# Optimization experiments

Hardware: AMD Instinct MI355X
Metric: run time of the kernel (lower is better)

Reference implementation:

```python
import jax, jax.numpy as jnp
import numpy as np

WS = 7        # window_size
SHIFT = 3     # shift_size
HEADS = 6
DIM = 192
HIDDEN = DIM * 6  # mlp_ratio=6
EPS = 1e-5


def _rel_pos_index(ws):
    # static relative-position index, (ws*ws, ws*ws) int
    coords = np.stack(np.meshgrid(np.arange(ws), np.arange(ws), indexing='ij')).reshape(2, -1)
    rel = coords[:, :, None] - coords[:, None, :]            # (2, N, N)
    rel = rel.transpose(1, 2, 0)                             # (N, N, 2)
    rel[:, :, 0] += ws - 1
    rel[:, :, 1] += ws - 1
    rel[:, :, 0] *= 2 * ws - 1
    return rel.sum(-1)


def _layernorm(t, g, b):
    m = t.mean(-1, keepdims=True)
    v = jnp.mean((t - m) ** 2, axis=-1, keepdims=True)
    return (t - m) * jax.lax.rsqrt(v + EPS) * g + b


def setup_inputs() -> dict:
    key = jax.random.key(0)
    ks = jax.random.split(key, 8)
    B, H, W = 16, 56, 56
    x = jax.random.normal(ks[0], (B, H * W, DIM), dtype=jnp.float32)
    p = lambda k, s: (jax.random.normal(k, s, dtype=jnp.float32) * 0.02)
    return {
        'x': x, 'H': H, 'W': W,
        'ln1_g': jnp.ones((DIM,), jnp.float32), 'ln1_b': jnp.zeros((DIM,), jnp.float32),
        'qkv_w': p(ks[1], (3 * DIM, DIM)), 'qkv_b': jnp.zeros((3 * DIM,), jnp.float32),
        'rpb': p(ks[2], ((2 * WS - 1) ** 2, HEADS)),
        'proj_w': p(ks[3], (DIM, DIM)), 'proj_b': jnp.zeros((DIM,), jnp.float32),
        'ln2_g': jnp.ones((DIM,), jnp.float32), 'ln2_b': jnp.zeros((DIM,), jnp.float32),
        'fc1_w': p(ks[4], (HIDDEN, DIM)), 'fc1_b': jnp.zeros((HIDDEN,), jnp.float32),
        'fc2_w': p(ks[5], (DIM, HIDDEN)), 'fc2_b': jnp.zeros((DIM,), jnp.float32),
    }


def reference(x, H, W, ln1_g, ln1_b, qkv_w, qkv_b, rpb, proj_w, proj_b,
              ln2_g, ln2_b, fc1_w, fc1_b, fc2_w, fc2_b):
    B, L, C = x.shape
    hd = C // HEADS
    shortcut = x
    h = _layernorm(x, ln1_g, ln1_b).reshape(B, H, W, C)
    pad_r = (WS - W % WS) % WS
    pad_b = (WS - H % WS) % WS
    h = jnp.pad(h, ((0, 0), (0, pad_b), (0, pad_r), (0, 0)))
    Hp, Wp = H + pad_b, W + pad_r
    if SHIFT > 0:
        h = jnp.roll(h, (-SHIFT, -SHIFT), axis=(1, 2))
    # window partition -> (nW*B, WS*WS, C)
    h = h.reshape(B, Hp // WS, WS, Wp // WS, WS, C).transpose(0, 1, 3, 2, 4, 5)
    h = h.reshape(-1, WS * WS, C)
    nB, N, _ = h.shape
    qkv = (h @ qkv_w.T + qkv_b).reshape(nB, N, 3, HEADS, hd).transpose(2, 0, 3, 1, 4)
    q, k, v = qkv[0], qkv[1], qkv[2]       # (nB, heads, N, hd)
    scale = hd ** -0.5
    attn = jnp.einsum('bhnd,bhmd->bhnm', q * scale, k)
    idx = _rel_pos_index(WS)
    bias = rpb[idx.reshape(-1)].reshape(N, N, HEADS).transpose(2, 0, 1)  # (heads, N, N)
    attn = jax.nn.softmax(attn + bias[None], axis=-1)
    out = jnp.einsum('bhnm,bhmd->bhnd', attn, v).transpose(0, 2, 1, 3).reshape(nB, N, C)
    out = out @ proj_w.T + proj_b
    # window reverse -> (B, Hp, Wp, C)
    out = out.reshape(B, Hp // WS, Wp // WS, WS, WS, C).transpose(0, 1, 3, 2, 4, 5)
    out = out.reshape(B, Hp, Wp, C)
    if SHIFT > 0:
        out = jnp.roll(out, (SHIFT, SHIFT), axis=(1, 2))
    out = out[:, :H, :W, :].reshape(B, H * W, C)
    x = shortcut + out
    h2 = _layernorm(x, ln2_g, ln2_b)
    h2 = jax.nn.gelu(h2 @ fc1_w.T + fc1_b, approximate=False)
    return x + (h2 @ fc2_w.T + fc2_b)
```

## Files before the change

kernel.cpp:

```cpp
#include <hip/hip_runtime.h>

typedef unsigned short u16;
typedef __bf16 bf16x8 __attribute__((ext_vector_type(8)));
typedef float f32x4 __attribute__((ext_vector_type(4)));

__device__ __forceinline__ u16 f2bf(float f) {
  union { float f; unsigned int u; } v; v.f = f;
  unsigned int u = v.u;
  u += 0x7fffu + ((u >> 16) & 1u);
  return (u16)(u >> 16);
}
__device__ __forceinline__ float bf2f(u16 h) {
  union { unsigned int u; float f; } v; v.u = ((unsigned int)h) << 16; return v.f;
}

__global__ __launch_bounds__(256) void cast_weights(
    const float* __restrict__ w0, const float* __restrict__ w1,
    const float* __restrict__ w2, const float* __restrict__ w3,
    u16* __restrict__ o0, u16* __restrict__ o1,
    u16* __restrict__ o2, u16* __restrict__ o3) {
  int i = blockIdx.x * 256 + threadIdx.x;
  if (i < 110592) o0[i] = f2bf(w0[i]);
  if (i < 36864)  o1[i] = f2bf(w1[i]);
  if (i < 221184) o2[i] = f2bf(w2[i]);
  if (i < 221184) o3[i] = f2bf(w3[i]);
}

__global__ __launch_bounds__(256) void ln_kernel(
    const float* __restrict__ x, const float* __restrict__ g,
    const float* __restrict__ b, u16* __restrict__ out) {
  int row = blockIdx.x * 4 + (threadIdx.x >> 6);
  int lane = threadIdx.x & 63;
  const float* xr = x + (long)row * 192;
  float e0 = xr[lane], e1 = xr[lane + 64], e2 = xr[lane + 128];
  float s = e0 + e1 + e2;
  #pragma unroll
  for (int o = 1; o < 64; o <<= 1) s += __shfl_xor(s, o);
  float mean = s * (1.0f / 192.0f);
  float d0 = e0 - mean, d1 = e1 - mean, d2 = e2 - mean;
  float q = d0 * d0 + d1 * d1 + d2 * d2;
  #pragma unroll
  for (int o = 1; o < 64; o <<= 1) q += __shfl_xor(q, o);
  float rstd = rsqrtf(q * (1.0f / 192.0f) + 1e-5f);
  u16* orow = out + (long)row * 192;
  orow[lane]       = f2bf(d0 * rstd * g[lane]       + b[lane]);
  orow[lane + 64]  = f2bf(d1 * rstd * g[lane + 64]  + b[lane + 64]);
  orow[lane + 128] = f2bf(d2 * rstd * g[lane + 128] + b[lane + 128]);
}

template<int MODE>
__global__ __launch_bounds__(256) void gemm_kernel(
    const u16* __restrict__ A, const u16* __restrict__ W,
    const float* __restrict__ bias, const float* __restrict__ resid,
    void* __restrict__ out, int N, int K) {
  __shared__ u16 lA[128 * 40];
  __shared__ u16 lB[64 * 40];
  int tid = threadIdx.x;
  int wave = tid >> 6, lane = tid & 63;
  int wm = wave >> 1, wn = wave & 1;
  int quad = lane >> 4, l15 = lane & 15;
  long bm = (long)blockIdx.x * 128;
  int bn = blockIdx.y * 64;
  int r = tid >> 2, cg = (tid & 3) * 8;
  f32x4 acc[4][2] = {};
  for (int k0 = 0; k0 < K; k0 += 32) {
    uint4 a0 = *(const uint4*)(A + (bm + r) * K + k0 + cg);
    uint4 a1 = *(const uint4*)(A + (bm + 64 + r) * K + k0 + cg);
    uint4 b0 = *(const uint4*)(W + (long)(bn + r) * K + k0 + cg);
    __syncthreads();
    *(uint4*)&lA[r * 40 + cg] = a0;
    *(uint4*)&lA[(64 + r) * 40 + cg] = a1;
    *(uint4*)&lB[r * 40 + cg] = b0;
    __syncthreads();
    bf16x8 af[4], bfr[2];
    #pragma unroll
    for (int mt = 0; mt < 4; mt++)
      af[mt] = *(const bf16x8*)&lA[(wm * 64 + mt * 16 + l15) * 40 + quad * 8];
    #pragma unroll
    for (int nt = 0; nt < 2; nt++)
      bfr[nt] = *(const bf16x8*)&lB[(wn * 32 + nt * 16 + l15) * 40 + quad * 8];
    #pragma unroll
    for (int mt = 0; mt < 4; mt++)
      #pragma unroll
      for (int nt = 0; nt < 2; nt++)
        acc[mt][nt] = __builtin_amdgcn_mfma_f32_16x16x32_bf16(af[mt], bfr[nt], acc[mt][nt], 0, 0, 0);
  }
  #pragma unroll
  for (int mt = 0; mt < 4; mt++) {
    #pragma unroll
    for (int nt = 0; nt < 2; nt++) {
      int col = bn + wn * 32 + nt * 16 + l15;
      float bi = bias[col];
      #pragma unroll
      for (int j = 0; j < 4; j++) {
        long row = bm + wm * 64 + mt * 16 + quad * 4 + j;
        float v = acc[mt][nt][j] + bi;
        long idx = row * N + col;
        if (MODE == 0) {
          ((u16*)out)[idx] = f2bf(v);
        } else if (MODE == 1) {
          v = 0.5f * v * (1.0f + erff(v * 0.70710678118f));
          ((u16*)out)[idx] = f2bf(v);
        } else {
          ((float*)out)[idx] = resid[idx] + v;
        }
      }
    }
  }
}

__global__ __launch_bounds__(256) void attn_kernel(
    const u16* __restrict__ qkv, const float* __restrict__ rpb,
    u16* __restrict__ attn) {
  __shared__ float ql[49 * 36], kl[49 * 36], vl[49 * 36];
  __shared__ float S[49 * 52];
  __shared__ int rowmap[49];
  int tid = threadIdx.x;
  int win = blockIdx.x, head = blockIdx.y;
  int b = win >> 6, wy = (win >> 3) & 7, wx = win & 7;
  if (tid < 49) {
    int i = tid / 7, j = tid - i * 7;
    int y  = (wy * 7 + i + 3) % 56;
    int xx = (wx * 7 + j + 3) % 56;
    rowmap[tid] = b * 3136 + y * 56 + xx;
  }
  __syncthreads();
  const float scale = 0.17677669529663687f;
  for (int t = tid; t < 49 * 32; t += 256) {
    int n = t >> 5, d = t & 31;
    long base = (long)rowmap[n] * 576 + head * 32 + d;
    ql[n * 36 + d] = bf2f(qkv[base]) * scale;
    kl[n * 36 + d] = bf2f(qkv[base + 192]);
    vl[n * 36 + d] = bf2f(qkv[base + 384]);
  }
  __syncthreads();
  for (int e = tid; e < 49 * 49; e += 256) {
    int n = e / 49, m = e - n * 49;
    const float4* qp = (const float4*)&ql[n * 36];
    const float4* kp = (const float4*)&kl[m * 36];
    float s = 0.0f;
    #pragma unroll
    for (int d4 = 0; d4 < 8; d4++) {
      float4 a = qp[d4], bb = kp[d4];
      s += a.x * bb.x + a.y * bb.y + a.z * bb.z + a.w * bb.w;
    }
    int ni = n / 7, nj = n - ni * 7, mi = m / 7, mj = m - mi * 7;
    s += rpb[((ni - mi + 6) * 13 + (nj - mj + 6)) * 6 + head];
    S[n * 52 + m] = s;
  }
  __syncthreads();
  if (tid < 49) {
    float mx = -1e30f;
    for (int m = 0; m < 49; m++) mx = fmaxf(mx, S[tid * 52 + m]);
    float sum = 0.0f;
    for (int m = 0; m < 49; m++) {
      float e = __expf(S[tid * 52 + m] - mx);
      S[tid * 52 + m] = e; sum += e;
    }
    float inv = 1.0f / sum;
    for (int m = 0; m < 49; m++) S[tid * 52 + m] *= inv;
  }
  __syncthreads();
  for (int e = tid; e < 49 * 8; e += 256) {
    int n = e >> 3, d4 = (e & 7) * 4;
    float4 o = make_float4(0.f, 0.f, 0.f, 0.f);
    for (int m = 0; m < 49; m++) {
      float p = S[n * 52 + m];
      const float4 vv = *(const float4*)&vl[m * 36 + d4];
      o.x += p * vv.x; o.y += p * vv.y; o.z += p * vv.z; o.w += p * vv.w;
    }
    long gb = (long)rowmap[n] * 192 + head * 32 + d4;
    unsigned int p0 = (unsigned int)f2bf(o.x) | ((unsigned int)f2bf(o.y) << 16);
    unsigned int p1 = (unsigned int)f2bf(o.z) | ((unsigned int)f2bf(o.w) << 16);
    *(uint2*)&attn[gb] = make_uint2(p0, p1);
  }
}

extern "C" void kernel_launch(void* const* d_in, const int* in_sizes, int n_in,
                              void* d_out, int out_size, void* d_ws, size_t ws_size,
                              hipStream_t stream) {
  (void)in_sizes; (void)n_in; (void)out_size; (void)ws_size;
  const float* x      = (const float*)d_in[0];
  const float* ln1_g  = (const float*)d_in[3];
  const float* ln1_b  = (const float*)d_in[4];
  const float* qkv_w  = (const float*)d_in[5];
  const float* qkv_b  = (const float*)d_in[6];
  const float* rpb    = (const float*)d_in[7];
  const float* proj_w = (const float*)d_in[8];
  const float* proj_b = (const float*)d_in[9];
  const float* ln2_g  = (const float*)d_in[10];
  const float* ln2_b  = (const float*)d_in[11];
  const float* fc1_w  = (const float*)d_in[12];
  const float* fc1_b  = (const float*)d_in[13];
  const float* fc2_w  = (const float*)d_in[14];
  const float* fc2_b  = (const float*)d_in[15];

  char* ws = (char*)d_ws;
  float* x2   = (float*)(ws + 0);
  u16* hA     = (u16*)(ws + 38535168);
  u16* qkv    = (u16*)(ws + 57802752);
  u16* attn   = (u16*)(ws + 115605504);
  u16* hid    = (u16*)(ws + 57802752);
  u16* wbuf   = (u16*)(ws + 173408256);
  u16* qkv_wb = wbuf;
  u16* proj_wb = wbuf + 110592;
  u16* fc1_wb = wbuf + 147456;
  u16* fc2_wb = wbuf + 368640;

  cast_weights<<<dim3(864), 256, 0, stream>>>(qkv_w, proj_w, fc1_w, fc2_w,
                                              qkv_wb, proj_wb, fc1_wb, fc2_wb);
  ln_kernel<<<dim3(12544), 256, 0, stream>>>(x, ln1_g, ln1_b, hA);
  gemm_kernel<0><<<dim3(392, 9), 256, 0, stream>>>(hA, qkv_wb, qkv_b, nullptr,
                                                   qkv, 576, 192);
  attn_kernel<<<dim3(1024, 6), 256, 0, stream>>>(qkv, rpb, attn);
  gemm_kernel<2><<<dim3(392, 3), 256, 0, stream>>>(attn, proj_wb, proj_b, x,
                                                   x2, 192, 192);
  ln_kernel<<<dim3(12544), 256, 0, stream>>>(x2, ln2_g, ln2_b, hA);
  gemm_kernel<1><<<dim3(392, 18), 256, 0, stream>>>(hA, fc1_wb, fc1_b, nullptr,
                                                    hid, 1152, 192);
  gemm_kernel<2><<<dim3(392, 3), 256, 0, stream>>>(hid, fc2_wb, fc2_b, x2,
                                                   (float*)d_out, 192, 1152);
}
```

Baseline: 374.3 us.

## Rewrite window attention with MFMA per wave, precompute bias table, widen fc1 tiles

The window attention kernel now gives each wave one (window, head) pair. It computes QK^T and PV with bf16 MFMA instructions on tiles padded to 64, replacing the scalar fp32 dot products and the single-thread softmax. A small kernel precomputes a padded relative-position bias table per head, with -1e30 in the padded key slots, so the attention kernel no longer gathers rpb. The GEMM is templated on tile counts, and fc1 uses a 128x128 tile to halve its grid. Probabilities and V are kept in bf16, which lowers precision relative to the fp32 softmax path.

```diff
diff --git a/kernel.cpp b/kernel.cpp
--- a/kernel.cpp
+++ b/kernel.cpp
@@ -26,6 +26,23 @@
   if (i < 221184) o3[i] = f2bf(w3[i]);
 }
 
+__global__ __launch_bounds__(256) void build_btab(
+    const float* __restrict__ rpb, float* __restrict__ btab) {
+  int id = blockIdx.x * 256 + threadIdx.x;
+  int head = id >> 12;
+  int m = (id >> 6) & 63;
+  int r = id & 63;
+  float v;
+  if (m >= 49) v = -1e30f;
+  else if (r >= 49) v = 0.0f;
+  else {
+    int mi = m / 7, mj = m - mi * 7;
+    int ri = r / 7, rj = r - ri * 7;
+    v = rpb[((ri - mi + 6) * 13 + (rj - mj + 6)) * 6 + head];
+  }
+  btab[id] = v;
+}
+
 __global__ __launch_bounds__(256) void ln_kernel(
     const float* __restrict__ x, const float* __restrict__ g,
     const float* __restrict__ b, u16* __restrict__ out) {
@@ -48,52 +65,57 @@
   orow[lane + 128] = f2bf(d2 * rstd * g[lane + 128] + b[lane + 128]);
 }
 
-template<int MODE>
+template<int MODE, int MT, int NT>
 __global__ __launch_bounds__(256) void gemm_kernel(
     const u16* __restrict__ A, const u16* __restrict__ W,
     const float* __restrict__ bias, const float* __restrict__ resid,
     void* __restrict__ out, int N, int K) {
-  __shared__ u16 lA[128 * 40];
-  __shared__ u16 lB[64 * 40];
+  __shared__ u16 lA[MT * 32 * 40];
+  __shared__ u16 lB[NT * 32 * 40];
   int tid = threadIdx.x;
   int wave = tid >> 6, lane = tid & 63;
   int wm = wave >> 1, wn = wave & 1;
   int quad = lane >> 4, l15 = lane & 15;
-  long bm = (long)blockIdx.x * 128;
-  int bn = blockIdx.y * 64;
+  long bm = (long)blockIdx.x * (MT * 32);
+  int bn = blockIdx.y * (NT * 32);
   int r = tid >> 2, cg = (tid & 3) * 8;
-  f32x4 acc[4][2] = {};
+  f32x4 acc[MT][NT] = {};
   for (int k0 = 0; k0 < K; k0 += 32) {
-    uint4 a0 = *(const uint4*)(A + (bm + r) * K + k0 + cg);
-    uint4 a1 = *(const uint4*)(A + (bm + 64 + r) * K + k0 + cg);
-    uint4 b0 = *(const uint4*)(W + (long)(bn + r) * K + k0 + cg);
+    uint4 av[MT / 2], bv[NT / 2];
+    #pragma unroll
+    for (int i = 0; i < MT / 2; i++)
+      av[i] = *(const uint4*)(A + (bm + i * 64 + r) * K + k0 + cg);
+    #pragma unroll
+    for (int i = 0; i < NT / 2; i++)
+      bv[i] = *(const uint4*)(W + (long)(bn + i * 64 + r) * K + k0 + cg);
     __syncthreads();
-    *(uint4*)&lA[r * 40 + cg] = a0;
-    *(uint4*)&lA[(64 + r) * 40 + cg] = a1;
-    *(uint4*)&lB[r * 40 + cg] = b0;
+    #pragma unroll
+    for (int i = 0; i < MT / 2; i++) *(uint4*)&lA[(i * 64 + r) * 40 + cg] = av[i];
+    #pragma unroll
+    for (int i = 0; i < NT / 2; i++) *(uint4*)&lB[(i * 64 + r) * 40 + cg] = bv[i];
     __syncthreads();
-    bf16x8 af[4], bfr[2];
-    #pragma unroll
-    for (int mt = 0; mt < 4; mt++)
-      af[mt] = *(const bf16x8*)&lA[(wm * 64 + mt * 16 + l15) * 40 + quad * 8];
-    #pragma unroll
-    for (int nt = 0; nt < 2; nt++)
-      bfr[nt] = *(const bf16x8*)&lB[(wn * 32 + nt * 16 + l15) * 40 + quad * 8];
-    #pragma unroll
-    for (int mt = 0; mt < 4; mt++)
+    bf16x8 af[MT], bfr[NT];
+    #pragma unroll
+    for (int mt = 0; mt < MT; mt++)
+      af[mt] = *(const bf16x8*)&lA[(wm * (MT * 16) + mt * 16 + l15) * 40 + quad * 8];
+    #pragma unroll
+    for (int nt = 0; nt < NT; nt++)
+      bfr[nt] = *(const bf16x8*)&lB[(wn * (NT * 16) + nt * 16 + l15) * 40 + quad * 8];
+    #pragma unroll
+    for (int mt = 0; mt < MT; mt++)
       #pragma unroll
-      for (int nt = 0; nt < 2; nt++)
+      for (int nt = 0; nt < NT; nt++)
         acc[mt][nt] = __builtin_amdgcn_mfma_f32_16x16x32_bf16(af[mt], bfr[nt], acc[mt][nt], 0, 0, 0);
   }
   #pragma unroll
-  for (int mt = 0; mt < 4; mt++) {
-    #pragma unroll
-    for (int nt = 0; nt < 2; nt++) {
-      int col = bn + wn * 32 + nt * 16 + l15;
+  for (int mt = 0; mt < MT; mt++) {
+    #pragma unroll
+    for (int nt = 0; nt < NT; nt++) {
+      int col = bn + wn * (NT * 16) + nt * 16 + l15;
       float bi = bias[col];
       #pragma unroll
       for (int j = 0; j < 4; j++) {
-        long row = bm + wm * 64 + mt * 16 + quad * 4 + j;
+        long row = bm + wm * (MT * 16) + mt * 16 + quad * 4 + j;
         float v = acc[mt][nt][j] + bi;
         long idx = row * N + col;
         if (MODE == 0) {
@@ -110,69 +132,134 @@
 }
 
 __global__ __launch_bounds__(256) void attn_kernel(
-    const u16* __restrict__ qkv, const float* __restrict__ rpb,
+    const u16* __restrict__ qkv, const float* __restrict__ btab,
     u16* __restrict__ attn) {
-  __shared__ float ql[49 * 36], kl[49 * 36], vl[49 * 36];
-  __shared__ float S[49 * 52];
-  __shared__ int rowmap[49];
+  __shared__ u16 lds[4 * 7552];
   int tid = threadIdx.x;
-  int win = blockIdx.x, head = blockIdx.y;
+  int wave = tid >> 6, lane = tid & 63;
+  int quad = lane >> 4, l15 = lane & 15;
+  int w = blockIdx.x * 4 + wave;
+  int win = w / 6, head = w - win * 6;
   int b = win >> 6, wy = (win >> 3) & 7, wx = win & 7;
-  if (tid < 49) {
-    int i = tid / 7, j = tid - i * 7;
-    int y  = (wy * 7 + i + 3) % 56;
-    int xx = (wx * 7 + j + 3) % 56;
-    rowmap[tid] = b * 3136 + y * 56 + xx;
+  u16* lq = lds + wave * 7552;
+  u16* lk = lq + 2560;
+  u16* lvt = lq + 5120;
+  float* rsum = (float*)(lq + 7424);
+  u16* lp = lq;
+
+  #pragma unroll
+  for (int p = 0; p < 4; p++) {
+    int n = p * 16 + (lane >> 2);
+    int qtr = (lane & 3) * 8;
+    uint4 qv = {}, kv = {}, vv = {};
+    if (n < 49) {
+      int i = n / 7, j = n - i * 7;
+      int y = wy * 7 + i + 3;  if (y >= 56) y -= 56;
+      int xx = wx * 7 + j + 3; if (xx >= 56) xx -= 56;
+      long base = ((long)(b * 3136 + y * 56 + xx)) * 576 + head * 32 + qtr;
+      qv = *(const uint4*)(qkv + base);
+      kv = *(const uint4*)(qkv + base + 192);
+      vv = *(const uint4*)(qkv + base + 384);
+    }
+    *(uint4*)&lq[n * 40 + qtr] = qv;
+    *(uint4*)&lk[n * 40 + qtr] = kv;
+    const u16* vp = (const u16*)&vv;
+    #pragma unroll
+    for (int d = 0; d < 8; d++) lvt[(qtr + d) * 72 + n] = vp[d];
   }
   __syncthreads();
+
+  bf16x8 ka[4], qb[4];
+  #pragma unroll
+  for (int t = 0; t < 4; t++) {
+    ka[t] = *(const bf16x8*)&lk[(t * 16 + l15) * 40 + quad * 8];
+    qb[t] = *(const bf16x8*)&lq[(t * 16 + l15) * 40 + quad * 8];
+  }
+  f32x4 s[4][4];
+  const f32x4 fz = {0.0f, 0.0f, 0.0f, 0.0f};
+  #pragma unroll
+  for (int tm = 0; tm < 4; tm++)
+    #pragma unroll
+    for (int tr = 0; tr < 4; tr++)
+      s[tm][tr] = __builtin_amdgcn_mfma_f32_16x16x32_bf16(ka[tm], qb[tr], fz, 0, 0, 0);
+
   const float scale = 0.17677669529663687f;
-  for (int t = tid; t < 49 * 32; t += 256) {
-    int n = t >> 5, d = t & 31;
-    long base = (long)rowmap[n] * 576 + head * 32 + d;
-    ql[n * 36 + d] = bf2f(qkv[base]) * scale;
-    kl[n * 36 + d] = bf2f(qkv[base + 192]);
-    vl[n * 36 + d] = bf2f(qkv[base + 384]);
+  const float* bt = btab + head * 4096;
+  float mx[4] = {-1e30f, -1e30f, -1e30f, -1e30f};
+  #pragma unroll
+  for (int tm = 0; tm < 4; tm++) {
+    int m0 = tm * 16 + quad * 4;
+    #pragma unroll
+    for (int tr = 0; tr < 4; tr++) {
+      int r = tr * 16 + l15;
+      #pragma unroll
+      for (int j = 0; j < 4; j++) {
+        float v = s[tm][tr][j] * scale + bt[(m0 + j) * 64 + r];
+        s[tm][tr][j] = v;
+        mx[tr] = fmaxf(mx[tr], v);
+      }
+    }
+  }
+  #pragma unroll
+  for (int tr = 0; tr < 4; tr++) {
+    mx[tr] = fmaxf(mx[tr], __shfl_xor(mx[tr], 16));
+    mx[tr] = fmaxf(mx[tr], __shfl_xor(mx[tr], 32));
+  }
+  float sm[4] = {0.f, 0.f, 0.f, 0.f};
+  #pragma unroll
+  for (int tm = 0; tm < 4; tm++) {
+    #pragma unroll
+    for (int tr = 0; tr < 4; tr++) {
+      int r = tr * 16 + l15;
+      float e0 = __expf(s[tm][tr][0] - mx[tr]);
+      float e1 = __expf(s[tm][tr][1] - mx[tr]);
+      float e2 = __expf(s[tm][tr][2] - mx[tr]);
+      float e3 = __expf(s[tm][tr][3] - mx[tr]);
+      sm[tr] += (e0 + e1) + (e2 + e3);
+      uint2 pk;
+      pk.x = (unsigned int)f2bf(e0) | ((unsigned int)f2bf(e1) << 16);
+      pk.y = (unsigned int)f2bf(e2) | ((unsigned int)f2bf(e3) << 16);
+      *(uint2*)&lp[r * 72 + tm * 16 + quad * 4] = pk;
+    }
+  }
+  #pragma unroll
+  for (int tr = 0; tr < 4; tr++) {
+    sm[tr] += __shfl_xor(sm[tr], 16);
+    sm[tr] += __shfl_xor(sm[tr], 32);
+  }
+  if (quad == 0) {
+    #pragma unroll
+    for (int tr = 0; tr < 4; tr++) rsum[tr * 16 + l15] = 1.0f / sm[tr];
   }
   __syncthreads();
-  for (int e = tid; e < 49 * 49; e += 256) {
-    int n = e / 49, m = e - n * 49;
-    const float4* qp = (const float4*)&ql[n * 36];
-    const float4* kp = (const float4*)&kl[m * 36];
-    float s = 0.0f;
-    #pragma unroll
-    for (int d4 = 0; d4 < 8; d4++) {
-      float4 a = qp[d4], bb = kp[d4];
-      s += a.x * bb.x + a.y * bb.y + a.z * bb.z + a.w * bb.w;
-    }
-    int ni = n / 7, nj = n - ni * 7, mi = m / 7, mj = m - mi * 7;
-    s += rpb[((ni - mi + 6) * 13 + (nj - mj + 6)) * 6 + head];
-    S[n * 52 + m] = s;
-  }
-  __syncthreads();
-  if (tid < 49) {
-    float mx = -1e30f;
-    for (int m = 0; m < 49; m++) mx = fmaxf(mx, S[tid * 52 + m]);
-    float sum = 0.0f;
-    for (int m = 0; m < 49; m++) {
-      float e = __expf(S[tid * 52 + m] - mx);
-      S[tid * 52 + m] = e; sum += e;
-    }
-    float inv = 1.0f / sum;
-    for (int m = 0; m < 49; m++) S[tid * 52 + m] *= inv;
-  }
-  __syncthreads();
-  for (int e = tid; e < 49 * 8; e += 256) {
-    int n = e >> 3, d4 = (e & 7) * 4;
-    float4 o = make_float4(0.f, 0.f, 0.f, 0.f);
-    for (int m = 0; m < 49; m++) {
-      float p = S[n * 52 + m];
-      const float4 vv = *(const float4*)&vl[m * 36 + d4];
-      o.x += p * vv.x; o.y += p * vv.y; o.z += p * vv.z; o.w += p * vv.w;
-    }
-    long gb = (long)rowmap[n] * 192 + head * 32 + d4;
-    unsigned int p0 = (unsigned int)f2bf(o.x) | ((unsigned int)f2bf(o.y) << 16);
-    unsigned int p1 = (unsigned int)f2bf(o.z) | ((unsigned int)f2bf(o.w) << 16);
-    *(uint2*)&attn[gb] = make_uint2(p0, p1);
+
+  f32x4 o[4][2] = {};
+  #pragma unroll
+  for (int ks = 0; ks < 2; ks++) {
+    bf16x8 vb0 = *(const bf16x8*)&lvt[(l15) * 72 + ks * 32 + quad * 8];
+    bf16x8 vb1 = *(const bf16x8*)&lvt[(16 + l15) * 72 + ks * 32 + quad * 8];
+    #pragma unroll
+    for (int rt = 0; rt < 4; rt++) {
+      bf16x8 pf = *(const bf16x8*)&lp[(rt * 16 + l15) * 72 + ks * 32 + quad * 8];
+      o[rt][0] = __builtin_amdgcn_mfma_f32_16x16x32_bf16(pf, vb0, o[rt][0], 0, 0, 0);
+      o[rt][1] = __builtin_amdgcn_mfma_f32_16x16x32_bf16(pf, vb1, o[rt][1], 0, 0, 0);
+    }
+  }
+  #pragma unroll
+  for (int rt = 0; rt < 4; rt++) {
+    #pragma unroll
+    for (int j = 0; j < 4; j++) {
+      int r = rt * 16 + quad * 4 + j;
+      if (r < 49) {
+        float inv = rsum[r];
+        int i = r / 7, jj = r - i * 7;
+        int y = wy * 7 + i + 3;   if (y >= 56) y -= 56;
+        int xx = wx * 7 + jj + 3; if (xx >= 56) xx -= 56;
+        long base = ((long)(b * 3136 + y * 56 + xx)) * 192 + head * 32 + l15;
+        attn[base]      = f2bf(o[rt][0][j] * inv);
+        attn[base + 16] = f2bf(o[rt][1][j] * inv);
+      }
+    }
   }
 }
 
@@ -198,26 +285,28 @@
   char* ws = (char*)d_ws;
   float* x2   = (float*)(ws + 0);
   u16* hA     = (u16*)(ws + 38535168);
+  float* btab = (float*)(ws + 38535168);
   u16* qkv    = (u16*)(ws + 57802752);
   u16* attn   = (u16*)(ws + 115605504);
   u16* hid    = (u16*)(ws + 57802752);
   u16* wbuf   = (u16*)(ws + 173408256);
-  u16* qkv_wb = wbuf;
+  u16* qkv_wb  = wbuf;
   u16* proj_wb = wbuf + 110592;
-  u16* fc1_wb = wbuf + 147456;
-  u16* fc2_wb = wbuf + 368640;
+  u16* fc1_wb  = wbuf + 147456;
+  u16* fc2_wb  = wbuf + 368640;
 
   cast_weights<<<dim3(864), 256, 0, stream>>>(qkv_w, proj_w, fc1_w, fc2_w,
                                               qkv_wb, proj_wb, fc1_wb, fc2_wb);
   ln_kernel<<<dim3(12544), 256, 0, stream>>>(x, ln1_g, ln1_b, hA);
-  gemm_kernel<0><<<dim3(392, 9), 256, 0, stream>>>(hA, qkv_wb, qkv_b, nullptr,
-                                                   qkv, 576, 192);
-  attn_kernel<<<dim3(1024, 6), 256, 0, stream>>>(qkv, rpb, attn);
-  gemm_kernel<2><<<dim3(392, 3), 256, 0, stream>>>(attn, proj_wb, proj_b, x,
-                                                   x2, 192, 192);
+  gemm_kernel<0, 4, 2><<<dim3(392, 9), 256, 0, stream>>>(hA, qkv_wb, qkv_b, nullptr,
+                                                         qkv, 576, 192);
+  build_btab<<<dim3(96), 256, 0, stream>>>(rpb, btab);
+  attn_kernel<<<dim3(1536), 256, 0, stream>>>(qkv, btab, attn);
+  gemm_kernel<2, 4, 2><<<dim3(392, 3), 256, 0, stream>>>(attn, proj_wb, proj_b, x,
+                                                         x2, 192, 192);
   ln_kernel<<<dim3(12544), 256, 0, stream>>>(x2, ln2_g, ln2_b, hA);
-  gemm_kernel<1><<<dim3(392, 18), 256, 0, stream>>>(hA, fc1_wb, fc1_b, nullptr,
-                                                    hid, 1152, 192);
-  gemm_kernel<2><<<dim3(392, 3), 256, 0, stream>>>(hid, fc2_wb, fc2_b, x2,
-                                                   (float*)d_out, 192, 1152);
-}
+  gemm_kernel<1, 4, 4><<<dim3(392, 9), 256, 0, stream>>>(hA, fc1_wb, fc1_b, nullptr,
+                                                         hid, 1152, 192);
+  gemm_kernel<2, 4, 2><<<dim3(392, 3), 256, 0, stream>>>(hid, fc2_wb, fc2_b, x2,
+                                                         (float*)d_out, 192, 1152);
+}
```

Measured after the change: 506.9 us. +35.4%, slower.
